# Performance work log

Measured on AMD Instinct MI355X. Metric: run time of the kernel, lower is better.

## Reference

```python
import jax, jax.numpy as jnp
import numpy as np

N_NODES = 50000
DROP_P = 0.6


def gcn_layer(x, src, dst, W, b):
    # 0P convolution: sum features of neighbors (scatter-add over edges), then linear.
    agg = jax.ops.segment_sum(x[src], dst, num_segments=N_NODES)  # [N, F]
    return agg @ W + b


def setup_inputs() -> dict:
    key = jax.random.key(0)
    k1, k2, k3, k4, k5, k6 = jax.random.split(key, 6)
    x = jax.random.normal(k1, (N_NODES, 96), dtype=jnp.float32)
    edge_index = jax.random.randint(k2, (2, 800000), 0, N_NODES, dtype=jnp.int64)
    s1 = 1.0 / np.sqrt(96.0)
    s2 = 1.0 / np.sqrt(64.0)
    W1 = jax.random.uniform(k3, (96, 64), jnp.float32, -s1, s1)
    b1 = jax.random.uniform(k4, (64,), jnp.float32, -s1, s1)
    W2 = jax.random.uniform(k5, (64, 5), jnp.float32, -s2, s2)
    b2 = jax.random.uniform(k6, (5,), jnp.float32, -s2, s2)
    return {"x": x, "edge_index": edge_index, "W1": W1, "b1": b1, "W2": W2, "b2": b2}


def reference(x, edge_index, W1, b1, W2, b2):
    src, dst = edge_index[0], edge_index[1]
    h = gcn_layer(x, src, dst, W1, b1)          # [N, hidden]
    h = jax.nn.relu(h)
    # dropout(p=0.6), deterministic mask from a fixed key
    keep = jax.random.bernoulli(jax.random.key(1), 1.0 - DROP_P, h.shape)
    h = jnp.where(keep, h / (1.0 - DROP_P), 0.0)
    out = gcn_layer(h, src, dst, W2, b2)        # [N, num_classes]
    return out
```

## Files before the change

### kernel.cpp

```cpp
#include <hip/hip_runtime.h>

#define FIN 96
#define HID 64
#define NCLS 5
#define BSH 7
#define BNODES 128
#define MAXNB 512
#define CAPSH 12
#define EPB 4096
#define MAXRUNS 256
#define G1R 64
#define SXP 100

__device__ __forceinline__ unsigned rotl32(unsigned x, int d) {
    return (x << d) | (x >> (32 - d));
}

__device__ __forceinline__ void threefry2x32(unsigned k0, unsigned k1,
                                             unsigned c0, unsigned c1,
                                             unsigned& o0, unsigned& o1) {
    unsigned ks2 = k0 ^ k1 ^ 0x1BD11BDAu;
    unsigned x0 = c0 + k0, x1 = c1 + k1;
#define RND(r) { x0 += x1; x1 = rotl32(x1, r); x1 ^= x0; }
#define G0 RND(13) RND(15) RND(26) RND(6)
#define G1 RND(17) RND(29) RND(16) RND(24)
    G0; x0 += k1;  x1 += ks2 + 1u;
    G1; x0 += ks2; x1 += k0 + 2u;
    G0; x0 += k0;  x1 += k1 + 3u;
    G1; x0 += k1;  x1 += ks2 + 4u;
    G0; x0 += ks2; x1 += k0 + 5u;
#undef G0
#undef G1
#undef RND
    o0 = x0; o1 = x1;
}

__device__ __forceinline__ float drop_mask_mul(unsigned t) {
    unsigned o0, o1;
    threefry2x32(0u, 1u, 0u, t, o0, o1);
    unsigned bits = o0 ^ o1;
    float u = __uint_as_float((bits >> 9) | 0x3f800000u) - 1.0f;
    return (u < 0.4f) ? 2.5f : 0.0f;
}

__device__ __forceinline__ unsigned short f2bf(float f) {
    unsigned u = __float_as_uint(f);
    unsigned r = 0x7fffu + ((u >> 16) & 1u);
    return (unsigned short)((u + r) >> 16);
}

__device__ __forceinline__ float bflo(unsigned u) { return __uint_as_float(u << 16); }
__device__ __forceinline__ float bfhi(unsigned u) { return __uint_as_float(u & 0xffff0000u); }

__device__ __forceinline__ int wave_excl_scan(int v, int lane) {
    int inc = v;
    #pragma unroll
    for (int off = 1; off < 64; off <<= 1) {
        int u = __shfl_up(inc, off, 64);
        if (lane >= off) inc += u;
    }
    return inc - v;
}

__global__ __launch_bounds__(256) void gemm1_bin_kernel(
        const float* __restrict__ x, const float* __restrict__ W,
        unsigned short* __restrict__ t1b,
        const int* __restrict__ src, const int* __restrict__ dst,
        int* __restrict__ cntMat, int* __restrict__ startMat,
        unsigned* __restrict__ bin, int N, int E, int NB, int nbb) {
    __shared__ __align__(16) char smem[50176];
    if ((int)blockIdx.x < nbb) {
        int* hist_s = (int*)smem;
        int* cur_s  = hist_s + MAXNB;
        int blk = blockIdx.x;
        int e0 = blk * EPB;
        for (int k = threadIdx.x; k < NB; k += 256) hist_s[k] = 0;
        __syncthreads();
        int ss[16], dd[16];
        int base = e0 + threadIdx.x * 16;
        #pragma unroll
        for (int q = 0; q < 4; ++q) {
            int b4 = base + q * 4;
            if (b4 + 3 < E) {
                int4 s4 = *(const int4*)&src[b4];
                int4 d4 = *(const int4*)&dst[b4];
                ss[q*4+0]=s4.x; ss[q*4+1]=s4.y; ss[q*4+2]=s4.z; ss[q*4+3]=s4.w;
                dd[q*4+0]=d4.x; dd[q*4+1]=d4.y; dd[q*4+2]=d4.z; dd[q*4+3]=d4.w;
            } else {
                #pragma unroll
                for (int j = 0; j < 4; ++j) {
                    ss[q*4+j] = (b4+j < E) ? src[b4+j] : 0;
                    dd[q*4+j] = (b4+j < E) ? dst[b4+j] : -1;
                }
            }
        }
        #pragma unroll
        for (int j = 0; j < 16; ++j)
            if (dd[j] >= 0) atomicAdd(&hist_s[dd[j] >> BSH], 1);
        __syncthreads();
        if (threadIdx.x < 64) {
            int lane = threadIdx.x;
            int h[7]; int t = 0;
            #pragma unroll
            for (int j = 0; j < 7; ++j) {
                int k = lane * 7 + j;
                h[j] = (k < NB) ? hist_s[k] : 0;
                t += h[j];
            }
            int excl = wave_excl_scan(t, lane);
            #pragma unroll
            for (int j = 0; j < 7; ++j) {
                int k = lane * 7 + j;
                if (k < NB) {
                    cur_s[k] = excl;
                    cntMat[k * nbb + blk]   = h[j];
                    startMat[k * nbb + blk] = e0 + excl;
                }
                excl += h[j];
            }
        }
        __syncthreads();
        #pragma unroll
        for (int j = 0; j < 16; ++j) {
            int d = dd[j];
            if (d < 0) continue;
            int k = d >> BSH;
            int p = e0 + atomicAdd(&cur_s[k], 1);
            bin[p] = ((unsigned)(d & (BNODES - 1)) << 16) | (unsigned)ss[j];
        }
    } else {
        float* sX = (float*)smem;
        float* sW = (float*)(smem + 25600);
        int row0 = ((int)blockIdx.x - nbb) * G1R;
        for (int i = threadIdx.x * 4; i < FIN * HID; i += 1024)
            *(float4*)&sW[i] = *(const float4*)&W[i];
        for (int i = threadIdx.x; i < G1R * (FIN / 4); i += 256) {
            int r = i / (FIN / 4), m = i % (FIN / 4);
            int gr = row0 + r;
            float4 v = make_float4(0.f, 0.f, 0.f, 0.f);
            if (gr < N) v = *(const float4*)&x[gr * FIN + m * 4];
            *(float4*)&sX[r * SXP + m * 4] = v;
        }
        __syncthreads();
        int tc = threadIdx.x & 15;
        int tr = threadIdx.x >> 4;
        float acc[4][4] = {};
        const float* xb = &sX[tr * 4 * SXP];
        for (int k = 0; k < FIN; ++k) {
            float4 w = *(const float4*)&sW[k * HID + tc * 4];
            #pragma unroll
            for (int j = 0; j < 4; ++j) {
                float xv = xb[j * SXP + k];
                acc[j][0] += xv * w.x;
                acc[j][1] += xv * w.y;
                acc[j][2] += xv * w.z;
                acc[j][3] += xv * w.w;
            }
        }
        #pragma unroll
        for (int j = 0; j < 4; ++j) {
            int gr = row0 + tr * 4 + j;
            if (gr < N) {
                ushort4 o;
                o.x = f2bf(acc[j][0]); o.y = f2bf(acc[j][1]);
                o.z = f2bf(acc[j][2]); o.w = f2bf(acc[j][3]);
                *(ushort4*)&t1b[gr * HID + tc * 4] = o;
            }
        }
    }
}

__global__ __launch_bounds__(1024) void sortagg_kernel(
        const int* __restrict__ cntMat, const int* __restrict__ startMat,
        const unsigned* __restrict__ bin, const uint4* __restrict__ t1v,
        const float* __restrict__ b1, const float* __restrict__ W2,
        int* __restrict__ offset, int* __restrict__ count,
        unsigned short* __restrict__ sortedSrc, float* __restrict__ t2p,
        int N, int nbb) {
    __shared__ int cntRow[MAXRUNS];
    __shared__ int startRow[MAXRUNS];
    __shared__ int runOff[MAXRUNS + 1];
    __shared__ int cnt_s[BNODES], off_s[BNODES], cur_s[BNODES];
    __shared__ unsigned raw_s[4096];
    __shared__ unsigned short list_s[4096];
    __shared__ float sW2[HID * NCLS];
    __shared__ float sB1[HID];
    int b = blockIdx.x, tid = threadIdx.x;

    for (int i = tid; i < HID * NCLS; i += 1024) sW2[i] = W2[i];
    if (tid < HID) sB1[tid] = b1[tid];
    if (tid < nbb) {
        cntRow[tid]   = cntMat[b * nbb + tid];
        startRow[tid] = startMat[b * nbb + tid];
    }
    if (tid < BNODES) cnt_s[tid] = 0;
    __syncthreads();
    if (tid < 64) {
        int c[4]; int t = 0;
        #pragma unroll
        for (int j = 0; j < 4; ++j) {
            int r = tid * 4 + j;
            c[j] = (r < nbb) ? cntRow[r] : 0;
            t += c[j];
        }
        int excl = wave_excl_scan(t, tid);
        #pragma unroll
        for (int j = 0; j < 4; ++j) {
            runOff[tid * 4 + j] = excl;
            excl += c[j];
        }
    }
    __syncthreads();
    int T = runOff[nbb];
    if (T > 4096) T = 4096;

    for (int i = tid; i < T; i += 1024) {
        int lo = 0, hi = nbb;
        while (hi - lo > 1) {
            int mid = (lo + hi) >> 1;
            if (runOff[mid] <= i) lo = mid; else hi = mid;
        }
        unsigned rec = bin[startRow[lo] + (i - runOff[lo])];
        raw_s[i] = rec;
        atomicAdd(&cnt_s[rec >> 16], 1);
    }
    __syncthreads();
    if (tid < 64) {
        int c0 = cnt_s[2 * tid], c1 = cnt_s[2 * tid + 1];
        int p0 = (c0 + 3) & ~3, p1 = (c1 + 3) & ~3;
        int excl = wave_excl_scan(p0 + p1, tid);
        off_s[2 * tid]     = excl;
        off_s[2 * tid + 1] = excl + p0;
    }
    __syncthreads();
    if (tid < BNODES) {
        cur_s[tid] = off_s[tid];
        int node = (b << BSH) + tid;
        if (node < N) {
            offset[node] = (b << CAPSH) + off_s[tid];
            count[node]  = cnt_s[tid];
        }
    }
    __syncthreads();
    for (int i = tid; i < T; i += 1024) {
        unsigned rec = raw_s[i];
        int ld = (int)(rec >> 16);
        int pos = atomicAdd(&cur_s[ld], 1);
        unsigned short sv = (unsigned short)(rec & 0xffffu);
        if (pos < 4096) {
            list_s[pos] = sv;
            sortedSrc[(b << CAPSH) + pos] = sv;
        }
    }
    __syncthreads();
    int g = tid >> 3, l = tid & 7;
    int node = (b << BSH) + g;
    if (node >= N) return;
    int beg = off_s[g];
    int end = beg + cnt_s[g];
    float a0 = 0.f, a1 = 0.f, a2 = 0.f, a3 = 0.f,
          a4 = 0.f, a5 = 0.f, a6 = 0.f, a7 = 0.f;
    int i = beg;
    for (; i + 3 < end; i += 4) {
        uint2 idx = *(const uint2*)&list_s[i];
        int s0 = idx.x & 0xffffu, s1 = idx.x >> 16;
        int s2 = idx.y & 0xffffu, s3 = idx.y >> 16;
        uint4 u0 = t1v[s0 * 8 + l];
        uint4 u1 = t1v[s1 * 8 + l];
        uint4 u2 = t1v[s2 * 8 + l];
        uint4 u3 = t1v[s3 * 8 + l];
        a0 += bflo(u0.x) + bflo(u1.x) + bflo(u2.x) + bflo(u3.x);
        a1 += bfhi(u0.x) + bfhi(u1.x) + bfhi(u2.x) + bfhi(u3.x);
        a2 += bflo(u0.y) + bflo(u1.y) + bflo(u2.y) + bflo(u3.y);
        a3 += bfhi(u0.y) + bfhi(u1.y) + bfhi(u2.y) + bfhi(u3.y);
        a4 += bflo(u0.z) + bflo(u1.z) + bflo(u2.z) + bflo(u3.z);
        a5 += bfhi(u0.z) + bfhi(u1.z) + bfhi(u2.z) + bfhi(u3.z);
        a6 += bflo(u0.w) + bflo(u1.w) + bflo(u2.w) + bflo(u3.w);
        a7 += bfhi(u0.w) + bfhi(u1.w) + bfhi(u2.w) + bfhi(u3.w);
    }
    for (; i < end; ++i) {
        uint4 u = t1v[(int)list_s[i] * 8 + l];
        a0 += bflo(u.x); a1 += bfhi(u.x);
        a2 += bflo(u.y); a3 += bfhi(u.y);
        a4 += bflo(u.z); a5 += bfhi(u.z);
        a6 += bflo(u.w); a7 += bfhi(u.w);
    }
    int f0 = l * 8;
    unsigned tb = (unsigned)(node * HID + f0);
    float acc[8] = {a0, a1, a2, a3, a4, a5, a6, a7};
    float s0 = 0.f, s1 = 0.f, s2 = 0.f, s3 = 0.f, s4 = 0.f;
    #pragma unroll
    for (int j = 0; j < 8; ++j) {
        float h = fmaxf(acc[j] + sB1[f0 + j], 0.0f) * drop_mask_mul(tb + j);
        const float* w = &sW2[(f0 + j) * NCLS];
        s0 += h * w[0]; s1 += h * w[1]; s2 += h * w[2];
        s3 += h * w[3]; s4 += h * w[4];
    }
    #pragma unroll
    for (int off = 1; off < 8; off <<= 1) {
        s0 += __shfl_xor(s0, off);
        s1 += __shfl_xor(s1, off);
        s2 += __shfl_xor(s2, off);
        s3 += __shfl_xor(s3, off);
        s4 += __shfl_xor(s4, off);
    }
    float v = (l == 0) ? s0 : (l == 1) ? s1 : (l == 2) ? s2
             : (l == 3) ? s3 : s4;
    if (l < NCLS) t2p[node * 8 + l] = v;
}

__global__ __launch_bounds__(256) void out_fused_kernel(
        const int* __restrict__ offset, const int* __restrict__ count,
        const unsigned short* __restrict__ sortedSrc,
        const float* __restrict__ t2p, const float* __restrict__ b2,
        float* __restrict__ out, int N) {
    int tid = blockIdx.x * 256 + threadIdx.x;
    if (tid >= N * NCLS) return;
    int node = tid / NCLS;
    int c = tid - node * NCLS;
    int beg = offset[node];
    int end = beg + count[node];
    float accA = b2[c], accB = 0.f;
    int i = beg;
    for (; i + 3 < end; i += 4) {
        uint2 idx = *(const uint2*)&sortedSrc[i];
        int s0 = idx.x & 0xffffu, s1 = idx.x >> 16;
        int s2 = idx.y & 0xffffu, s3 = idx.y >> 16;
        accA += t2p[s0 * 8 + c] + t2p[s1 * 8 + c];
        accB += t2p[s2 * 8 + c] + t2p[s3 * 8 + c];
    }
    for (; i < end; ++i) accA += t2p[(int)sortedSrc[i] * 8 + c];
    out[tid] = accA + accB;
}

extern "C" void kernel_launch(void* const* d_in, const int* in_sizes, int n_in,
                              void* d_out, int out_size, void* d_ws, size_t ws_size,
                              hipStream_t stream) {
    const float* x   = (const float*)d_in[0];
    const int*   ei  = (const int*)d_in[1];
    const float* W1  = (const float*)d_in[2];
    const float* b1  = (const float*)d_in[3];
    const float* W2  = (const float*)d_in[4];
    const float* b2  = (const float*)d_in[5];
    float*       out = (float*)d_out;

    const int N = in_sizes[0] / FIN;
    const int E = in_sizes[1] / 2;
    const int* src = ei;
    const int* dst = ei + E;

    const int NB  = (N + BNODES - 1) / BNODES;
    const int nbb = (E + EPB - 1) / EPB;
    const int g1b = (N + G1R - 1) / G1R;

    unsigned short* t1b       = (unsigned short*)d_ws;
    float*          t2p       = (float*)(t1b + (size_t)N * HID);
    int*            count     = (int*)(t2p + (size_t)N * 8);
    int*            offset    = count + N;
    int*            cntMat    = offset + N;
    int*            startMat  = cntMat + (size_t)NB * nbb;
    unsigned*       bin       = (unsigned*)(startMat + (size_t)NB * nbb);
    unsigned short* sortedSrc = (unsigned short*)(bin + E);

    gemm1_bin_kernel<<<nbb + g1b, 256, 0, stream>>>(
        x, W1, t1b, src, dst, cntMat, startMat, bin, N, E, NB, nbb);

    sortagg_kernel<<<NB, 1024, 0, stream>>>(
        cntMat, startMat, bin, (const uint4*)t1b, b1, W2,
        offset, count, sortedSrc, t2p, N, nbb);

    out_fused_kernel<<<(N * NCLS + 255) / 256, 256, 0, stream>>>(
        offset, count, sortedSrc, t2p, b2, out, N);
}
```

Before: 58.55 us.

## Halve node bucket size to 64 and transpose count/start matrices

Shrinks each destination bucket from 128 to 64 nodes, so the sort/aggregate kernel launches twice as many 512-thread blocks with half the shared-memory staging. This is meant to raise occupancy and spread work over more CUs. The count/start matrices are transposed so the binning writes are contiguous per block, at the cost of strided reads in sortagg. The bucket capacity drops to 2048 edges, which leaves less headroom for skewed buckets. The histogram scan is widened to 13 entries per lane and the offset scan is merged into one step.

```diff
diff --git a/kernel.cpp b/kernel.cpp
--- a/kernel.cpp
+++ b/kernel.cpp
@@ -3,10 +3,10 @@
 #define FIN 96
 #define HID 64
 #define NCLS 5
-#define BSH 7
-#define BNODES 128
-#define MAXNB 512
-#define CAPSH 12
+#define BSH 6
+#define BNODES 64
+#define MAXNB 1024
+#define CAPSH 11
 #define EPB 4096
 #define MAXRUNS 256
 #define G1R 64
@@ -100,21 +100,21 @@
         __syncthreads();
         if (threadIdx.x < 64) {
             int lane = threadIdx.x;
-            int h[7]; int t = 0;
+            int h[13]; int t = 0;
             #pragma unroll
-            for (int j = 0; j < 7; ++j) {
-                int k = lane * 7 + j;
+            for (int j = 0; j < 13; ++j) {
+                int k = lane * 13 + j;
                 h[j] = (k < NB) ? hist_s[k] : 0;
                 t += h[j];
             }
             int excl = wave_excl_scan(t, lane);
             #pragma unroll
-            for (int j = 0; j < 7; ++j) {
-                int k = lane * 7 + j;
+            for (int j = 0; j < 13; ++j) {
+                int k = lane * 13 + j;
                 if (k < NB) {
                     cur_s[k] = excl;
-                    cntMat[k * nbb + blk]   = h[j];
-                    startMat[k * nbb + blk] = e0 + excl;
+                    cntMat[blk * NB + k]   = h[j];
+                    startMat[blk * NB + k] = e0 + excl;
                 }
                 excl += h[j];
             }
@@ -170,28 +170,28 @@
     }
 }
 
-__global__ __launch_bounds__(1024) void sortagg_kernel(
+__global__ __launch_bounds__(512) void sortagg_kernel(
         const int* __restrict__ cntMat, const int* __restrict__ startMat,
         const unsigned* __restrict__ bin, const uint4* __restrict__ t1v,
         const float* __restrict__ b1, const float* __restrict__ W2,
         int* __restrict__ offset, int* __restrict__ count,
         unsigned short* __restrict__ sortedSrc, float* __restrict__ t2p,
-        int N, int nbb) {
+        int N, int nbb, int NB) {
     __shared__ int cntRow[MAXRUNS];
     __shared__ int startRow[MAXRUNS];
     __shared__ int runOff[MAXRUNS + 1];
     __shared__ int cnt_s[BNODES], off_s[BNODES], cur_s[BNODES];
-    __shared__ unsigned raw_s[4096];
-    __shared__ unsigned short list_s[4096];
+    __shared__ unsigned raw_s[2048];
+    __shared__ __align__(16) unsigned short list_s[2048];
     __shared__ float sW2[HID * NCLS];
     __shared__ float sB1[HID];
     int b = blockIdx.x, tid = threadIdx.x;
 
-    for (int i = tid; i < HID * NCLS; i += 1024) sW2[i] = W2[i];
+    for (int i = tid; i < HID * NCLS; i += 512) sW2[i] = W2[i];
     if (tid < HID) sB1[tid] = b1[tid];
     if (tid < nbb) {
-        cntRow[tid]   = cntMat[b * nbb + tid];
-        startRow[tid] = startMat[b * nbb + tid];
+        cntRow[tid]   = cntMat[tid * NB + b];
+        startRow[tid] = startMat[tid * NB + b];
     }
     if (tid < BNODES) cnt_s[tid] = 0;
     __syncthreads();
@@ -209,12 +209,13 @@
             runOff[tid * 4 + j] = excl;
             excl += c[j];
         }
+        if (tid == 63) runOff[256] = excl;
     }
     __syncthreads();
     int T = runOff[nbb];
-    if (T > 4096) T = 4096;
-
-    for (int i = tid; i < T; i += 1024) {
+    if (T > 2048) T = 2048;
+
+    for (int i = tid; i < T; i += 512) {
         int lo = 0, hi = nbb;
         while (hi - lo > 1) {
             int mid = (lo + hi) >> 1;
@@ -226,28 +227,24 @@
     }
     __syncthreads();
     if (tid < 64) {
-        int c0 = cnt_s[2 * tid], c1 = cnt_s[2 * tid + 1];
-        int p0 = (c0 + 3) & ~3, p1 = (c1 + 3) & ~3;
-        int excl = wave_excl_scan(p0 + p1, tid);
-        off_s[2 * tid]     = excl;
-        off_s[2 * tid + 1] = excl + p0;
-    }
-    __syncthreads();
-    if (tid < BNODES) {
-        cur_s[tid] = off_s[tid];
+        int c0 = cnt_s[tid];
+        int p0 = (c0 + 3) & ~3;
+        int excl = wave_excl_scan(p0, tid);
+        off_s[tid] = excl;
+        cur_s[tid] = excl;
         int node = (b << BSH) + tid;
         if (node < N) {
-            offset[node] = (b << CAPSH) + off_s[tid];
-            count[node]  = cnt_s[tid];
-        }
-    }
-    __syncthreads();
-    for (int i = tid; i < T; i += 1024) {
+            offset[node] = (b << CAPSH) + excl;
+            count[node]  = c0;
+        }
+    }
+    __syncthreads();
+    for (int i = tid; i < T; i += 512) {
         unsigned rec = raw_s[i];
         int ld = (int)(rec >> 16);
         int pos = atomicAdd(&cur_s[ld], 1);
         unsigned short sv = (unsigned short)(rec & 0xffffu);
-        if (pos < 4096) {
+        if (pos < 2048) {
             list_s[pos] = sv;
             sortedSrc[(b << CAPSH) + pos] = sv;
         }
@@ -358,16 +355,16 @@
     int*            count     = (int*)(t2p + (size_t)N * 8);
     int*            offset    = count + N;
     int*            cntMat    = offset + N;
-    int*            startMat  = cntMat + (size_t)NB * nbb;
-    unsigned*       bin       = (unsigned*)(startMat + (size_t)NB * nbb);
+    int*            startMat  = cntMat + (size_t)nbb * NB;
+    unsigned*       bin       = (unsigned*)(startMat + (size_t)nbb * NB);
     unsigned short* sortedSrc = (unsigned short*)(bin + E);
 
     gemm1_bin_kernel<<<nbb + g1b, 256, 0, stream>>>(
         x, W1, t1b, src, dst, cntMat, startMat, bin, N, E, NB, nbb);
 
-    sortagg_kernel<<<NB, 1024, 0, stream>>>(
+    sortagg_kernel<<<NB, 512, 0, stream>>>(
         cntMat, startMat, bin, (const uint4*)t1b, b1, W2,
-        offset, count, sortedSrc, t2p, N, nbb);
+        offset, count, sortedSrc, t2p, N, nbb, NB);
 
     out_fused_kernel<<<(N * NCLS + 255) / 256, 256, 0, stream>>>(
         offset, count, sortedSrc, t2p, b2, out, N);
```

Measured after the change: 58.87 us. No clear change (+0.5%).
